# Performance work log

Measured on AMD Instinct MI355X. Metric: run time of the kernel, lower is better.

## Reference

```python
import jax, jax.numpy as jnp
import numpy as np
import math

B, T, C, H = 4, 2048, 1024, 16
HS = C // H
EPS = 1e-5


def layernorm(x, g, b):
    mu = jnp.mean(x, axis=-1, keepdims=True)
    var = jnp.var(x, axis=-1, keepdims=True)
    return (x - mu) * jax.lax.rsqrt(var + EPS) * g + b


def setup_inputs() -> dict:
    key = jax.random.key(0)
    ks = jax.random.split(key, 7)
    rn = lambda k, s: jax.random.normal(k, s, dtype=jnp.float32) * 0.02
    return {
        "x": jax.random.normal(ks[0], (B, T, C), dtype=jnp.float32),
        "mask": jnp.tril(jnp.ones((T, T), dtype=jnp.int32)),  # causal tril buffer
        "wq": rn(ks[1], (H, HS, C)),  # stacked per-head Linear weights [out,in]
        "wk": rn(ks[2], (H, HS, C)),
        "wv": rn(ks[3], (H, HS, C)),
        "ln1_g": jnp.ones((C,), jnp.float32),
        "ln1_b": jnp.zeros((C,), jnp.float32),
        "ln2_g": jnp.ones((C,), jnp.float32),
        "ln2_b": jnp.zeros((C,), jnp.float32),
        "w1": rn(ks[4], (4 * C, C)),
        "b1": jnp.zeros((4 * C,), jnp.float32),
        "w2": rn(ks[5], (C, 4 * C)),
        "b2": jnp.zeros((C,), jnp.float32),
    }


def reference(x, mask, wq, wk, wv, ln1_g, ln1_b, ln2_g, ln2_b, w1, b1, w2, b2):
    Bx, Tx, Cx = x.shape
    h = layernorm(x, ln1_g, ln1_b)
    # per-head projections, batched over heads: [B,H,T,HS]
    q = jnp.einsum('btc,hdc->bhtd', h, wq)
    k = jnp.einsum('btc,hdc->bhtd', h, wk)
    v = jnp.einsum('btc,hdc->bhtd', h, wv)
    scores = jnp.einsum('bhtd,bhsd->bhts', q, k) * (1.0 / math.sqrt(HS))
    scores = jnp.where(mask[None, None, :Tx, :Tx] == 0, -jnp.inf, scores)
    w = jax.nn.softmax(scores, axis=-1)
    attn = jnp.einsum('bhts,bhsd->bhtd', w, v)  # [B,H,T,HS]
    attn = attn.transpose(0, 2, 1, 3).reshape(Bx, Tx, Cx)  # concat heads
    x = x + attn
    h2 = layernorm(x, ln2_g, ln2_b)
    ff = jax.nn.silu(h2 @ w1.T + b1) @ w2.T + b2  # dropout = identity (eval)
    return x + ff
```

## Files before the change

kernel.cpp:

```cpp
#include <hip/hip_runtime.h>
#include <stdint.h>

#define Bb 4
#define Tt 2048
#define Cc 1024
#define Hh 16
#define HSs 64

typedef __attribute__((ext_vector_type(8))) __bf16 bf16x8;
typedef __attribute__((ext_vector_type(4))) float f32x4;

__device__ __forceinline__ ushort f2bf(float f){
  union { float f; uint u; } c; c.f = f;
  uint r = c.u + 0x7fffu + ((c.u >> 16) & 1u);
  return (ushort)(r >> 16);
}
__device__ __forceinline__ float bf2f(ushort u){
  union { uint u; float f; } c; c.u = ((uint)u) << 16; return c.f;
}

__device__ __forceinline__ void gload16(const void* g, void* l){
  __builtin_amdgcn_global_load_lds(
      (__attribute__((address_space(1))) void*)(g),
      (__attribute__((address_space(3))) void*)(l), 16, 0, 0);
}

__global__ __launch_bounds__(256) void cast_all_kernel(
    const float* __restrict__ wq, const float* __restrict__ wk,
    const float* __restrict__ wv, const float* __restrict__ w1,
    const float* __restrict__ w2, ushort* __restrict__ out){
  int i = (blockIdx.x * 256 + threadIdx.x) * 4;
  const float* src; int off;
  if      (i <  1048576){ src = wq; off = i; }
  else if (i <  2097152){ src = wk; off = i - 1048576; }
  else if (i <  3145728){ src = wv; off = i - 2097152; }
  else if (i <  7340032){ src = w1; off = i - 3145728; }
  else                  { src = w2; off = i - 7340032; }
  float4 v = *(const float4*)(src + off);
  ushort4 o; o.x = f2bf(v.x); o.y = f2bf(v.y); o.z = f2bf(v.z); o.w = f2bf(v.w);
  *(ushort4*)(out + i) = o;
}

__global__ __launch_bounds__(256) void add_p1_kernel(float* __restrict__ out,
                                                     const float* __restrict__ p1){
  for (int it = 0; it < 4; ++it){
    size_t i = ((size_t)it * 2048 * 256 + blockIdx.x * 256 + threadIdx.x) * 4;
    float4 o = *(const float4*)(out + i);
    float4 p = *(const float4*)(p1 + i);
    o.x += p.x; o.y += p.y; o.z += p.z; o.w += p.w;
    *(float4*)(out + i) = o;
  }
}

__global__ __launch_bounds__(256) void ln1_kernel(const float* __restrict__ x,
    const float* __restrict__ gw, const float* __restrict__ bw,
    ushort* __restrict__ hout){
  int row = blockIdx.x, tid = threadIdx.x;
  size_t base = (size_t)row * Cc + tid * 4;
  float4 xv = *(const float4*)(x + base);
  float s  = xv.x + xv.y + xv.z + xv.w;
  float ss = xv.x*xv.x + xv.y*xv.y + xv.z*xv.z + xv.w*xv.w;
  #pragma unroll
  for (int off = 1; off < 64; off <<= 1){ s += __shfl_xor(s, off); ss += __shfl_xor(ss, off); }
  __shared__ float red[8];
  int wid = tid >> 6, lane = tid & 63;
  if (lane == 0){ red[wid] = s; red[4 + wid] = ss; }
  __syncthreads();
  s  = red[0] + red[1] + red[2] + red[3];
  ss = red[4] + red[5] + red[6] + red[7];
  float mu = s * (1.0f / Cc);
  float rstd = rsqrtf(ss * (1.0f / Cc) - mu * mu + 1e-5f);
  float4 gv = *(const float4*)(gw + tid * 4);
  float4 bv = *(const float4*)(bw + tid * 4);
  ushort4 o;
  o.x = f2bf((xv.x - mu) * rstd * gv.x + bv.x);
  o.y = f2bf((xv.y - mu) * rstd * gv.y + bv.y);
  o.z = f2bf((xv.z - mu) * rstd * gv.z + bv.z);
  o.w = f2bf((xv.w - mu) * rstd * gv.w + bv.w);
  *(ushort4*)(hout + base) = o;
}

__global__ __launch_bounds__(256) void ln2_kernel(const float* __restrict__ x,
    const ushort* __restrict__ attnb,
    const float* __restrict__ gw, const float* __restrict__ bw,
    float* __restrict__ x2, ushort* __restrict__ hout){
  int row = blockIdx.x, tid = threadIdx.x;
  size_t base = (size_t)row * Cc + tid * 4;
  float4 xv = *(const float4*)(x + base);
  ushort4 av = *(const ushort4*)(attnb + base);
  xv.x += bf2f(av.x); xv.y += bf2f(av.y); xv.z += bf2f(av.z); xv.w += bf2f(av.w);
  *(float4*)(x2 + base) = xv;
  float s  = xv.x + xv.y + xv.z + xv.w;
  float ss = xv.x*xv.x + xv.y*xv.y + xv.z*xv.z + xv.w*xv.w;
  #pragma unroll
  for (int off = 1; off < 64; off <<= 1){ s += __shfl_xor(s, off); ss += __shfl_xor(ss, off); }
  __shared__ float red[8];
  int wid = tid >> 6, lane = tid & 63;
  if (lane == 0){ red[wid] = s; red[4 + wid] = ss; }
  __syncthreads();
  s  = red[0] + red[1] + red[2] + red[3];
  ss = red[4] + red[5] + red[6] + red[7];
  float mu = s * (1.0f / Cc);
  float rstd = rsqrtf(ss * (1.0f / Cc) - mu * mu + 1e-5f);
  float4 gv = *(const float4*)(gw + tid * 4);
  float4 bv = *(const float4*)(bw + tid * 4);
  ushort4 o;
  o.x = f2bf((xv.x - mu) * rstd * gv.x + bv.x);
  o.y = f2bf((xv.y - mu) * rstd * gv.y + bv.y);
  o.z = f2bf((xv.z - mu) * rstd * gv.z + bv.z);
  o.w = f2bf((xv.w - mu) * rstd * gv.w + bv.w);
  *(ushort4*)(hout + base) = o;
}

#define MFMA_QUAD(SI, QI, BQ) \
  { \
    _Pragma("unroll") \
    for (int mi = 0; mi < 4; ++mi){ \
      acc[(SI)*4+mi][(QI)*2+0] = __builtin_amdgcn_mfma_f32_16x16x32_bf16(af[mi][0], BQ[0][0], acc[(SI)*4+mi][(QI)*2+0], 0,0,0); \
      acc[(SI)*4+mi][(QI)*2+0] = __builtin_amdgcn_mfma_f32_16x16x32_bf16(af[mi][1], BQ[0][1], acc[(SI)*4+mi][(QI)*2+0], 0,0,0); \
      acc[(SI)*4+mi][(QI)*2+1] = __builtin_amdgcn_mfma_f32_16x16x32_bf16(af[mi][0], BQ[1][0], acc[(SI)*4+mi][(QI)*2+1], 0,0,0); \
      acc[(SI)*4+mi][(QI)*2+1] = __builtin_amdgcn_mfma_f32_16x16x32_bf16(af[mi][1], BQ[1][1], acc[(SI)*4+mi][(QI)*2+1], 0,0,0); \
    } \
  }

#define PH_SYNC_PRE()  { __builtin_amdgcn_sched_barrier(0); __builtin_amdgcn_s_barrier(); \
                         asm volatile("s_waitcnt lgkmcnt(0)" ::: "memory"); \
                         __builtin_amdgcn_sched_barrier(0); __builtin_amdgcn_s_setprio(1); }
#define PH_SYNC_POST() { __builtin_amdgcn_s_setprio(0); __builtin_amdgcn_sched_barrier(0); \
                         __builtin_amdgcn_s_barrier(); }

template<int MODE>
__device__ __forceinline__ void gemm256_body(
    const ushort* __restrict__ A, const ushort* __restrict__ Bw,
    int N, int K, int ldO,
    ushort* __restrict__ obf, float* __restrict__ of32,
    float* __restrict__ p1, const float* __restrict__ bias)
{
  __shared__ __align__(16) ushort lds[2][2][2][128 * 64];
  int tid = threadIdx.x, lane = tid & 63, wid = tid >> 6;
  int wm = wid >> 2, wn = wid & 3;
  int c = lane & 15, g = lane >> 4;

  int nwg = gridDim.x, bid = blockIdx.x;
  int wgid = (bid & 7) * (nwg >> 3) + (bid >> 3);
  int m0, n0, koff = 0;
  if (MODE == 3){
    int split = wgid >> 7, rem = wgid & 127;
    m0 = (rem >> 2) << 8; n0 = (rem & 3) << 8; koff = split << 11;
  } else {
    int nTn = N >> 8;
    m0 = (wgid / nTn) << 8; n0 = (wgid % nTn) << 8;
  }

  const ushort* Ag = A  + (size_t)m0 * K + koff;
  const ushort* Bg = Bw + (size_t)n0 * K + koff;

  auto stage = [&](const ushort* gbase, int t, int ab, int h){
    #pragma unroll
    for (int j = 0; j < 2; ++j){
      int d = j * 8192 + wid * 1024 + lane * 16;
      int row = d >> 7;
      int colb = (d & 127) ^ ((row & 7) << 4);
      gload16((const char*)gbase + ((size_t)(h * 128 + row) * K + t * 64) * 2 + colb,
              (char*)&lds[t & 1][ab][h][0] + j * 8192 + wid * 1024);
    }
  };

  f32x4 acc[8][4] = {};
  bf16x8 af[4][2], bq0[2][2], bq1[2][2];
  int nt = (MODE == 3) ? (K >> 7) : (K >> 6);

  stage(Ag, 0, 0, 0); stage(Ag, 0, 0, 1);
  stage(Bg, 0, 1, 0); stage(Bg, 0, 1, 1);
  stage(Bg, 1, 1, 0); stage(Bg, 1, 1, 1);
  asm volatile("s_waitcnt vmcnt(4)" ::: "memory");
  __builtin_amdgcn_sched_barrier(0);
  __builtin_amdgcn_s_barrier();

  for (int t = 0; t < nt; ++t){
    const char* Abuf = (const char*)&lds[t & 1][0][wm][0];
    const char* Bbuf = (const char*)&lds[t & 1][1][wn >> 1][0];
    int brow0 = (wn & 1) * 64;

    #pragma unroll
    for (int mi = 0; mi < 4; ++mi){
      int row = mi * 16 + c, sw = (row & 7) << 4;
      af[mi][0] = *(const bf16x8*)(Abuf + row * 128 + ((g * 16) ^ sw));
      af[mi][1] = *(const bf16x8*)(Abuf + row * 128 + ((64 + g * 16) ^ sw));
    }
    #pragma unroll
    for (int nj = 0; nj < 2; ++nj){
      int row = brow0 + nj * 16 + c, sw = (row & 7) << 4;
      bq0[nj][0] = *(const bf16x8*)(Bbuf + row * 128 + ((g * 16) ^ sw));
      bq0[nj][1] = *(const bf16x8*)(Bbuf + row * 128 + ((64 + g * 16) ^ sw));
    }
    if (t + 1 < nt) stage(Ag, t + 1, 0, 0);
    PH_SYNC_PRE();
    MFMA_QUAD(0, 0, bq0);
    PH_SYNC_POST();

    #pragma unroll
    for (int nj = 0; nj < 2; ++nj){
      int row = brow0 + 32 + nj * 16 + c, sw = (row & 7) << 4;
      bq1[nj][0] = *(const bf16x8*)(Bbuf + row * 128 + ((g * 16) ^ sw));
      bq1[nj][1] = *(const bf16x8*)(Bbuf + row * 128 + ((64 + g * 16) ^ sw));
    }
    if (t + 1 < nt) stage(Ag, t + 1, 0, 1);
    PH_SYNC_PRE();
    MFMA_QUAD(0, 1, bq1);
    PH_SYNC_POST();

    #pragma unroll
    for (int mi = 0; mi < 4; ++mi){
      int row = 64 + mi * 16 + c, sw = (row & 7) << 4;
      af[mi][0] = *(const bf16x8*)(Abuf + row * 128 + ((g * 16) ^ sw));
      af[mi][1] = *(const bf16x8*)(Abuf + row * 128 + ((64 + g * 16) ^ sw));
    }
    if (t + 2 < nt) stage(Bg, t + 2, 1, 0);
    PH_SYNC_PRE();
    MFMA_QUAD(1, 0, bq0);
    PH_SYNC_POST();

    if (t + 2 < nt){
      stage(Bg, t + 2, 1, 1);
      asm volatile("s_waitcnt vmcnt(4)" ::: "memory");
    } else {
      asm volatile("s_waitcnt vmcnt(0)" ::: "memory");
    }
    __builtin_amdgcn_sched_barrier(0);
    __builtin_amdgcn_s_barrier();
    __builtin_amdgcn_s_setprio(1);
    MFMA_QUAD(1, 1, bq1);
    PH_SYNC_POST();
  }

  #pragma unroll
  for (int mi = 0; mi < 8; ++mi){
    #pragma unroll
    for (int ni = 0; ni < 4; ++ni){
      #pragma unroll
      for (int r = 0; r < 4; ++r){
        float v = acc[mi][ni][r];
        int m = m0 + wm * 128 + mi * 16 + g * 4 + r;
        int n = n0 + wn * 64 + ni * 16 + c;
        if (MODE == 0){
          int which = n >> 10;
          int nn = n & 1023;
          int b = m >> 11, t = m & (Tt - 1);
          int h = nn >> 6, d = nn & 63;
          float vv = (which == 0) ? v * 0.125f : v;
          size_t base = (size_t)which * (size_t)(Bb * Tt * Cc);
          size_t idx = (which == 2)
              ? ((((size_t)(b * Hh + h)) * HSs + d) * Tt + t)
              : ((((size_t)(b * Hh + h)) * Tt + t) * HSs + d);
          obf[base + idx] = f2bf(vv);
        } else if (MODE == 1){
          v += bias[n];
          float sv = v / (1.0f + __expf(-v));
          obf[(size_t)m * ldO + n] = f2bf(sv);
        } else {
          size_t idx = (size_t)m * N + n;
          if (koff == 0) of32[idx] = of32[idx] + v + bias[n];
          else           p1[idx] = v;
        }
      }
    }
  }
}

__global__ __launch_bounds__(512, 2) void gemm_qkv_kernel(
    const ushort* __restrict__ A, const ushort* __restrict__ Bw, int N, int K,
    ushort* __restrict__ obf){
  gemm256_body<0>(A, Bw, N, K, 0, obf, nullptr, nullptr, nullptr);
}
__global__ __launch_bounds__(512, 2) void gemm_ffn1_kernel(
    const ushort* __restrict__ A, const ushort* __restrict__ Bw, int N, int K, int ldO,
    ushort* __restrict__ obf, const float* __restrict__ bias){
  gemm256_body<1>(A, Bw, N, K, ldO, obf, nullptr, nullptr, bias);
}
__global__ __launch_bounds__(512, 2) void gemm_ffn2_kernel(
    const ushort* __restrict__ A, const ushort* __restrict__ Bw, int N, int K,
    float* __restrict__ of32, float* __restrict__ p1, const float* __restrict__ bias){
  gemm256_body<3>(A, Bw, N, K, N, nullptr, of32, p1, bias);
}

__global__ __launch_bounds__(256, 2) void attn_kernel(
    const ushort* __restrict__ q, const ushort* __restrict__ k,
    const ushort* __restrict__ vt, ushort* __restrict__ attnb)
{
  __shared__ __align__(16) ushort Ksm[3][64 * 64];
  __shared__ __align__(16) ushort Vsm[3][64 * 64];
  __shared__ __align__(16) ushort Pl[4][32 * 64];

  int bh  = blockIdx.y;
  int p   = blockIdx.x;
  int tid = threadIdx.x, wid = tid >> 6, lane = tid & 63;
  int g = lane >> 4, c = lane & 15;
  int qbA = 15 - p, qbB = p;
  int q0A = qbA * 128 + wid * 32;
  int q0B = qbB * 128 + wid * 32;
  const ushort* Qb = q  + (size_t)bh * Tt * HSs;
  const ushort* Kb = k  + (size_t)bh * Tt * HSs;
  const ushort* Vt = vt + (size_t)bh * HSs * Tt;
  char* Pw = (char*)&Pl[wid][0];

  auto stageKV = [&](int bsel, int s0){
    #pragma unroll
    for (int half = 0; half < 2; ++half){
      int i = wid + half * 4;
      int row = i * 8 + (lane >> 3);
      int col = ((lane & 7) ^ (row & 7)) * 8;
      gload16(Kb + (size_t)(s0 + row) * HSs + col, &Ksm[bsel][i * 512]);
      gload16(Vt + (size_t)row * Tt + s0 + col,    &Vsm[bsel][i * 512]);
    }
  };

  bf16x8 qfA[2][2], qfB[2][2];
  #pragma unroll
  for (int mi = 0; mi < 2; ++mi)
    #pragma unroll
    for (int ks = 0; ks < 2; ++ks){
      qfA[mi][ks] = *(const bf16x8*)(Qb + (size_t)(q0A + mi * 16 + c) * HSs + ks * 32 + g * 8);
      qfB[mi][ks] = *(const bf16x8*)(Qb + (size_t)(q0B + mi * 16 + c) * HSs + ks * 32 + g * 8);
    }

  f32x4 oA[2][4] = {}, oB[2][4] = {};
  float mA[2][4], lA[2][4], mB[2][4], lB[2][4];
  #pragma unroll
  for (int mi = 0; mi < 2; ++mi)
    #pragma unroll
    for (int r = 0; r < 4; ++r){
      mA[mi][r] = -1e30f; lA[mi][r] = 0.f;
      mB[mi][r] = -1e30f; lB[mi][r] = 0.f;
    }

  auto computeTile = [&](bf16x8 (&qf)[2][2], f32x4 (&o)[2][4],
                         float (&mrow)[2][4], float (&lpart)[2][4],
                         int q0w, int s0, const char* Kbuf, const char* Vbuf){
    f32x4 S[2][4] = {};
    bf16x8 kf[4][2];
    #pragma unroll
    for (int ni = 0; ni < 4; ++ni)
      #pragma unroll
      for (int ks = 0; ks < 2; ++ks)
        kf[ni][ks] = *(const bf16x8*)(Kbuf + (ni * 16 + c) * 128 + (((ks * 4 + g) ^ (c & 7)) << 4));
    #pragma unroll
    for (int mi = 0; mi < 2; ++mi)
      #pragma unroll
      for (int ni = 0; ni < 4; ++ni)
        #pragma unroll
        for (int ks = 0; ks < 2; ++ks)
          S[mi][ni] = __builtin_amdgcn_mfma_f32_16x16x32_bf16(qf[mi][ks], kf[ni][ks], S[mi][ni], 0, 0, 0);

    if (s0 + 63 > q0w){
      #pragma unroll
      for (int mi = 0; mi < 2; ++mi)
        #pragma unroll
        for (int ni = 0; ni < 4; ++ni)
          #pragma unroll
          for (int r = 0; r < 4; ++r){
            int tl = q0w + mi * 16 + g * 4 + r, sl = s0 + ni * 16 + c;
            if (sl > tl) S[mi][ni][r] = -1e30f;
          }
    }

    float lmax[2][4], worst = -1e30f;
    #pragma unroll
    for (int mi = 0; mi < 2; ++mi)
      #pragma unroll
      for (int r = 0; r < 4; ++r){
        float a0 = fmaxf(S[mi][0][r], S[mi][1][r]);
        float a1 = fmaxf(S[mi][2][r], S[mi][3][r]);
        lmax[mi][r] = fmaxf(a0, a1);
        worst = fmaxf(worst, lmax[mi][r] - mrow[mi][r]);
      }
    if (!__all(worst <= 8.0f)){
      #pragma unroll
      for (int mi = 0; mi < 2; ++mi)
        #pragma unroll
        for (int r = 0; r < 4; ++r){
          float mx = lmax[mi][r];
          mx = fmaxf(mx, __shfl_xor(mx, 1));
          mx = fmaxf(mx, __shfl_xor(mx, 2));
          mx = fmaxf(mx, __shfl_xor(mx, 4));
          mx = fmaxf(mx, __shfl_xor(mx, 8));
          float mnew  = fmaxf(mrow[mi][r], mx);
          float alpha = __expf(mrow[mi][r] - mnew);
          lpart[mi][r] *= alpha;
          #pragma unroll
          for (int dt = 0; dt < 4; ++dt) o[mi][dt][r] *= alpha;
          mrow[mi][r] = mnew;
        }
    }
    #pragma unroll
    for (int mi = 0; mi < 2; ++mi)
      #pragma unroll
      for (int r = 0; r < 4; ++r){
        int row = mi * 16 + g * 4 + r;
        float mb = mrow[mi][r] * 1.44269504f;
        float pp[4];
        #pragma unroll
        for (int ni = 0; ni < 4; ++ni){
          pp[ni] = exp2f(__builtin_fmaf(S[mi][ni][r], 1.44269504f, -mb));
          *(ushort*)(Pw + row * 128 + (((ni * 32 + 2 * c) ^ ((row & 7) << 4)))) = f2bf(pp[ni]);
        }
        lpart[mi][r] += (pp[0] + pp[1]) + (pp[2] + pp[3]);
      }

    bf16x8 vf[4][2];
    #pragma unroll
    for (int dt = 0; dt < 4; ++dt)
      #pragma unroll
      for (int ks = 0; ks < 2; ++ks)
        vf[dt][ks] = *(const bf16x8*)(Vbuf + (dt * 16 + c) * 128 + (((ks * 4 + g) ^ (c & 7)) << 4));
    #pragma unroll
    for (int mi = 0; mi < 2; ++mi){
      #pragma unroll
      for (int ks = 0; ks < 2; ++ks){
        bf16x8 pf = *(const bf16x8*)(Pw + (mi * 16 + c) * 128 + ((((ks * 4 + g) ^ (c & 7)) << 4)));
        #pragma unroll
        for (int dt = 0; dt < 4; ++dt)
          o[mi][dt] = __builtin_amdgcn_mfma_f32_16x16x32_bf16(pf, vf[dt][ks], o[mi][dt], 0, 0, 0);
      }
    }
  };

  int nchA = 2 * qbA + 2;

  stageKV(0, 0);
  stageKV(1, 64);
  asm volatile("s_waitcnt vmcnt(4)" ::: "memory");
  __builtin_amdgcn_sched_barrier(0);
  __builtin_amdgcn_s_barrier();

  int bufC = 0;
  for (int ch = 0; ch < nchA; ++ch){
    int s0 = ch * 64;
    bool staged = (ch + 2 < nchA);
    if (staged) stageKV((bufC == 0) ? 2 : bufC - 1, s0 + 128);

    const char* Kbuf = (const char*)&Ksm[bufC][0];
    const char* Vbuf = (const char*)&Vsm[bufC][0];
    if (s0 <= q0A + 31)
      computeTile(qfA, oA, mA, lA, q0A, s0, Kbuf, Vbuf);
    if (s0 <= q0B + 31)
      computeTile(qfB, oB, mB, lB, q0B, s0, Kbuf, Vbuf);

    if (staged) asm volatile("s_waitcnt vmcnt(4)" ::: "memory");
    else        asm volatile("s_waitcnt vmcnt(0)" ::: "memory");
    __builtin_amdgcn_sched_barrier(0);
    __builtin_amdgcn_s_barrier();
    bufC = (bufC == 2) ? 0 : bufC + 1;
  }

  int b = bh >> 4, h = bh & 15;
  #pragma unroll
  for (int mi = 0; mi < 2; ++mi)
    #pragma unroll
    for (int r = 0; r < 4; ++r){
      float la = lA[mi][r];
      la += __shfl_xor(la, 1); la += __shfl_xor(la, 2);
      la += __shfl_xor(la, 4); la += __shfl_xor(la, 8);
      float lia = 1.0f / la;
      float lb = lB[mi][r];
      lb += __shfl_xor(lb, 1); lb += __shfl_xor(lb, 2);
      lb += __shfl_xor(lb, 4); lb += __shfl_xor(lb, 8);
      float lib = 1.0f / lb;
      #pragma unroll
      for (int dt = 0; dt < 4; ++dt){
        int tA = q0A + mi * 16 + g * 4 + r;
        int tB = q0B + mi * 16 + g * 4 + r;
        attnb[((size_t)(b * Tt + tA)) * Cc + h * HSs + dt * 16 + c] = f2bf(oA[mi][dt][r] * lia);
        attnb[((size_t)(b * Tt + tB)) * Cc + h * HSs + dt * 16 + c] = f2bf(oB[mi][dt][r] * lib);
      }
    }
}

extern "C" void kernel_launch(void* const* d_in, const int* in_sizes, int n_in,
                              void* d_out, int out_size, void* d_ws, size_t ws_size,
                              hipStream_t stream) {
  (void)in_sizes; (void)n_in; (void)out_size; (void)ws_size;
  const float* x    = (const float*)d_in[0];
  const float* wq   = (const float*)d_in[2];
  const float* wk   = (const float*)d_in[3];
  const float* wv   = (const float*)d_in[4];
  const float* ln1g = (const float*)d_in[5];
  const float* ln1b = (const float*)d_in[6];
  const float* ln2g = (const float*)d_in[7];
  const float* ln2b = (const float*)d_in[8];
  const float* w1   = (const float*)d_in[9];
  const float* b1   = (const float*)d_in[10];
  const float* w2   = (const float*)d_in[11];
  const float* b2   = (const float*)d_in[12];
  float* out = (float*)d_out;

  char* ws = (char*)d_ws;
  const size_t SZ_ACT = (size_t)Bb * Tt * Cc * 2;
  ushort* h1    = (ushort*)(ws);
  ushort* qbuf  = (ushort*)(ws + SZ_ACT);
  ushort* kbuf  = (ushort*)(ws + 2 * SZ_ACT);
  ushort* vbuf  = (ushort*)(ws + 3 * SZ_ACT);
  ushort* attnb = (ushort*)(ws + 4 * SZ_ACT);
  ushort* h2    = (ushort*)(ws + 5 * SZ_ACT);
  ushort* h3    = (ushort*)(ws + 6 * SZ_ACT);
  float*  p1    = (float*)(ws + SZ_ACT);
  char*   wsw   = ws + 6 * SZ_ACT + (size_t)Bb * Tt * 4 * Cc * 2;
  ushort* wqb = (ushort*)(wsw);
  ushort* w1b = (ushort*)(wsw + 3 * (size_t)Cc * Cc * 2);
  ushort* w2b = (ushort*)(wsw + 3 * (size_t)Cc * Cc * 2 + (size_t)4 * Cc * Cc * 2);

  cast_all_kernel<<<dim3(11264), 256, 0, stream>>>(wq, wk, wv, w1, w2, wqb);

  ln1_kernel<<<dim3(Bb * Tt), 256, 0, stream>>>(x, ln1g, ln1b, h1);

  gemm_qkv_kernel<<<dim3(32 * 12), 512, 0, stream>>>(h1, wqb, 3 * Cc, Cc, qbuf);

  attn_kernel<<<dim3(8, Bb * Hh), 256, 0, stream>>>(qbuf, kbuf, vbuf, attnb);

  ln2_kernel<<<dim3(Bb * Tt), 256, 0, stream>>>(x, attnb, ln2g, ln2b, out, h2);

  gemm_ffn1_kernel<<<dim3(32 * 8), 512, 0, stream>>>(h2, w1b,                      2048, Cc, 4 * Cc, h3,        b1);
  gemm_ffn1_kernel<<<dim3(32 * 8), 512, 0, stream>>>(h2, w1b + (size_t)2048 * Cc,  2048, Cc, 4 * Cc, h3 + 2048, b1 + 2048);
  gemm_ffn2_kernel<<<dim3(256), 512, 0, stream>>>(h3, w2b, Cc, 4 * Cc, out, p1, b2);
  add_p1_kernel<<<dim3(2048), 256, 0, stream>>>(out, p1);
}
```

Measured before the change: 411.4 us.

## Process attention KV in chunk pairs with 4-buffer ring; store split-K partial in bf16

The attention loop now stages two KV chunks at a time into a four-slot LDS ring and computes two tiles per barrier pair. This halves the number of block barriers per chunk at the cost of more LDS per block, which may reduce occupancy. Separately, the FFN2 split-K partial is stored and reloaded as bf16 instead of fp32, cutting that round-trip traffic but adding rounding error. The float-to-bf16 conversion is also simplified from round-to-nearest-even to round-half-up.

```diff
diff --git a/kernel.cpp b/kernel.cpp
--- a/kernel.cpp
+++ b/kernel.cpp
@@ -12,8 +12,7 @@
 
 __device__ __forceinline__ ushort f2bf(float f){
   union { float f; uint u; } c; c.f = f;
-  uint r = c.u + 0x7fffu + ((c.u >> 16) & 1u);
-  return (ushort)(r >> 16);
+  return (ushort)((c.u + 0x8000u) >> 16);
 }
 __device__ __forceinline__ float bf2f(ushort u){
   union { uint u; float f; } c; c.u = ((uint)u) << 16; return c.f;
@@ -42,12 +41,12 @@
 }
 
 __global__ __launch_bounds__(256) void add_p1_kernel(float* __restrict__ out,
-                                                     const float* __restrict__ p1){
+                                                     const ushort* __restrict__ p1b){
   for (int it = 0; it < 4; ++it){
     size_t i = ((size_t)it * 2048 * 256 + blockIdx.x * 256 + threadIdx.x) * 4;
     float4 o = *(const float4*)(out + i);
-    float4 p = *(const float4*)(p1 + i);
-    o.x += p.x; o.y += p.y; o.z += p.z; o.w += p.w;
+    ushort4 p = *(const ushort4*)(p1b + i);
+    o.x += bf2f(p.x); o.y += bf2f(p.y); o.z += bf2f(p.z); o.w += bf2f(p.w);
     *(float4*)(out + i) = o;
   }
 }
@@ -134,7 +133,7 @@
     const ushort* __restrict__ A, const ushort* __restrict__ Bw,
     int N, int K, int ldO,
     ushort* __restrict__ obf, float* __restrict__ of32,
-    float* __restrict__ p1, const float* __restrict__ bias)
+    ushort* __restrict__ p1b, const float* __restrict__ bias)
 {
   __shared__ __align__(16) ushort lds[2][2][2][128 * 64];
   int tid = threadIdx.x, lane = tid & 63, wid = tid >> 6;
@@ -261,7 +260,7 @@
         } else {
           size_t idx = (size_t)m * N + n;
           if (koff == 0) of32[idx] = of32[idx] + v + bias[n];
-          else           p1[idx] = v;
+          else           p1b[idx] = f2bf(v);
         }
       }
     }
@@ -280,16 +279,16 @@
 }
 __global__ __launch_bounds__(512, 2) void gemm_ffn2_kernel(
     const ushort* __restrict__ A, const ushort* __restrict__ Bw, int N, int K,
-    float* __restrict__ of32, float* __restrict__ p1, const float* __restrict__ bias){
-  gemm256_body<3>(A, Bw, N, K, N, nullptr, of32, p1, bias);
+    float* __restrict__ of32, ushort* __restrict__ p1b, const float* __restrict__ bias){
+  gemm256_body<3>(A, Bw, N, K, N, nullptr, of32, p1b, bias);
 }
 
 __global__ __launch_bounds__(256, 2) void attn_kernel(
     const ushort* __restrict__ q, const ushort* __restrict__ k,
     const ushort* __restrict__ vt, ushort* __restrict__ attnb)
 {
-  __shared__ __align__(16) ushort Ksm[3][64 * 64];
-  __shared__ __align__(16) ushort Vsm[3][64 * 64];
+  __shared__ __align__(16) ushort Ksm[4][64 * 64];
+  __shared__ __align__(16) ushort Vsm[4][64 * 64];
   __shared__ __align__(16) ushort Pl[4][32 * 64];
 
   int bh  = blockIdx.y;
@@ -429,28 +428,36 @@
 
   stageKV(0, 0);
   stageKV(1, 64);
-  asm volatile("s_waitcnt vmcnt(4)" ::: "memory");
-  __builtin_amdgcn_sched_barrier(0);
-  __builtin_amdgcn_s_barrier();
-
-  int bufC = 0;
-  for (int ch = 0; ch < nchA; ++ch){
-    int s0 = ch * 64;
+
+  for (int ch = 0; ch < nchA; ch += 2){
     bool staged = (ch + 2 < nchA);
-    if (staged) stageKV((bufC == 0) ? 2 : bufC - 1, s0 + 128);
-
-    const char* Kbuf = (const char*)&Ksm[bufC][0];
-    const char* Vbuf = (const char*)&Vsm[bufC][0];
-    if (s0 <= q0A + 31)
-      computeTile(qfA, oA, mA, lA, q0A, s0, Kbuf, Vbuf);
-    if (s0 <= q0B + 31)
-      computeTile(qfB, oB, mB, lB, q0B, s0, Kbuf, Vbuf);
-
-    if (staged) asm volatile("s_waitcnt vmcnt(4)" ::: "memory");
-    else        asm volatile("s_waitcnt vmcnt(0)" ::: "memory");
+    if (staged){
+      stageKV((ch + 2) & 3, (ch + 2) * 64);
+      stageKV((ch + 3) & 3, (ch + 3) * 64);
+      asm volatile("s_waitcnt vmcnt(8)" ::: "memory");
+    } else {
+      asm volatile("s_waitcnt vmcnt(0)" ::: "memory");
+    }
     __builtin_amdgcn_sched_barrier(0);
     __builtin_amdgcn_s_barrier();
-    bufC = (bufC == 2) ? 0 : bufC + 1;
+
+    {
+      int s0 = ch * 64;
+      const char* Kbuf = (const char*)&Ksm[ch & 3][0];
+      const char* Vbuf = (const char*)&Vsm[ch & 3][0];
+      if (s0 <= q0A + 31) computeTile(qfA, oA, mA, lA, q0A, s0, Kbuf, Vbuf);
+      if (s0 <= q0B + 31) computeTile(qfB, oB, mB, lB, q0B, s0, Kbuf, Vbuf);
+    }
+    {
+      int s0 = (ch + 1) * 64;
+      const char* Kbuf = (const char*)&Ksm[(ch + 1) & 3][0];
+      const char* Vbuf = (const char*)&Vsm[(ch + 1) & 3][0];
+      if (s0 <= q0A + 31) computeTile(qfA, oA, mA, lA, q0A, s0, Kbuf, Vbuf);
+      if (s0 <= q0B + 31) computeTile(qfB, oB, mB, lB, q0B, s0, Kbuf, Vbuf);
+    }
+
+    __builtin_amdgcn_sched_barrier(0);
+    __builtin_amdgcn_s_barrier();
   }
 
   int b = bh >> 4, h = bh & 15;
@@ -503,7 +510,7 @@
   ushort* attnb = (ushort*)(ws + 4 * SZ_ACT);
   ushort* h2    = (ushort*)(ws + 5 * SZ_ACT);
   ushort* h3    = (ushort*)(ws + 6 * SZ_ACT);
-  float*  p1    = (float*)(ws + SZ_ACT);
+  ushort* p1b   = (ushort*)(ws + SZ_ACT);
   char*   wsw   = ws + 6 * SZ_ACT + (size_t)Bb * Tt * 4 * Cc * 2;
   ushort* wqb = (ushort*)(wsw);
   ushort* w1b = (ushort*)(wsw + 3 * (size_t)Cc * Cc * 2);
@@ -521,6 +528,6 @@
 
   gemm_ffn1_kernel<<<dim3(32 * 8), 512, 0, stream>>>(h2, w1b,                      2048, Cc, 4 * Cc, h3,        b1);
   gemm_ffn1_kernel<<<dim3(32 * 8), 512, 0, stream>>>(h2, w1b + (size_t)2048 * Cc,  2048, Cc, 4 * Cc, h3 + 2048, b1 + 2048);
-  gemm_ffn2_kernel<<<dim3(256), 512, 0, stream>>>(h3, w2b, Cc, 4 * Cc, out, p1, b2);
-  add_p1_kernel<<<dim3(2048), 256, 0, stream>>>(out, p1);
-}
+  gemm_ffn2_kernel<<<dim3(256), 512, 0, stream>>>(h3, w2b, Cc, 4 * Cc, out, p1b, b2);
+  add_p1_kernel<<<dim3(2048), 256, 0, stream>>>(out, p1b);
+}
```

Measured after the change: 401.1 us. 1.03x faster.
